# Optimization experiments

Measured on AMD Instinct MI355X. Metric: run time of the kernel, lower is better.

Reference implementation:

```python
import jax, jax.numpy as jnp
from jax import lax
import numpy as np

B, L, V, E, D, NC = 2048, 128, 128, 32, 64, 10
COMMIT = 0.25


def conv1d(x, w, b, stride, pad):
    # x: [N,C,L], w: torch Conv1d weight [out,in,k]
    y = lax.conv_general_dilated(x, w, (stride,), [(pad, pad)],
                                 dimension_numbers=('NCH', 'OIH', 'NCH'))
    return y + b[None, :, None]


def convT1d(x, w, b, stride, pad):
    # torch ConvTranspose1d weight [in,out,k]; out_len=(in-1)*stride-2*pad+k
    k = w.shape[-1]
    wf = jnp.flip(w, -1).transpose(1, 0, 2)  # -> OIH
    y = lax.conv_general_dilated(x, wf, (1,), [(k - 1 - pad, k - 1 - pad)],
                                 lhs_dilation=(stride,),
                                 dimension_numbers=('NCH', 'OIH', 'NCH'))
    return y + b[None, :, None]


def setup_inputs() -> dict:
    key = jax.random.key(0)
    ks = jax.random.split(key, 16)
    p = lambda k, shp, s=0.05: (jax.random.normal(k, shp, dtype=jnp.float32) * s)
    return {
        'text_indices': jax.random.randint(ks[0], (B, L), 0, V),
        'emb': p(ks[1], (V, E)),
        'enc_w1': p(ks[2], (64, E, 3)), 'enc_b1': jnp.zeros((64,), jnp.float32),
        'enc_w2': p(ks[3], (64, 64, 3)), 'enc_b2': jnp.zeros((64,), jnp.float32),
        'enc_w3': p(ks[4], (D, 64, 3)), 'enc_b3': jnp.zeros((D,), jnp.float32),
        'codebook': jax.random.uniform(ks[5], (NC, D), jnp.float32, -1.0 / NC, 1.0 / NC),
        'dec_w1': p(ks[6], (D, 64, 3)), 'dec_b1': jnp.zeros((64,), jnp.float32),
        'dec_w2': p(ks[7], (64, 64, 4)), 'dec_b2': jnp.zeros((64,), jnp.float32),
        'dec_w3': p(ks[8], (64, E, 4)), 'dec_b3': jnp.zeros((E,), jnp.float32),
        'out_w': p(ks[9], (V, E)), 'out_b': jnp.zeros((V,), jnp.float32),
    }


def reference(text_indices, emb, enc_w1, enc_b1, enc_w2, enc_b2, enc_w3, enc_b3,
              codebook, dec_w1, dec_b1, dec_w2, dec_b2, dec_w3, dec_b3, out_w, out_b):
    # ---- encode ----
    x = emb[text_indices]                      # [B,L,E]
    x = x.transpose(0, 2, 1)                   # [B,E,L]
    x = jax.nn.relu(conv1d(x, enc_w1, enc_b1, 2, 1))   # [B,64,64]
    x = jax.nn.relu(conv1d(x, enc_w2, enc_b2, 2, 1))   # [B,64,32]
    x = conv1d(x, enc_w3, enc_b3, 1, 0)        # [B,D,30]
    enc = x.transpose(0, 2, 1)                 # [B,30,D]
    features = jnp.broadcast_to(enc[:, :, None, :], (x.shape[0], 30, 30, D))  # [B,30,30,D]

    # ---- VQ: cdist + argmin + gather ----
    flat = features.reshape(-1, D)             # [B*900,D]
    d2 = (jnp.sum(flat * flat, axis=1, keepdims=True)
          - 2.0 * flat @ codebook.T
          + jnp.sum(codebook * codebook, axis=1)[None, :])  # [B*900,NC]
    codes = jnp.argmin(d2, axis=-1)
    puzzles = codes.reshape(features.shape[:-1])            # [B,30,30]
    quantized = codebook[codes].reshape(features.shape)     # [B,30,30,D]
    commitment_loss = jnp.mean((features - lax.stop_gradient(quantized)) ** 2)
    embedding_loss = jnp.mean((quantized - lax.stop_gradient(features)) ** 2)
    vq_loss = embedding_loss + COMMIT * commitment_loss
    quantized_st = features + lax.stop_gradient(quantized - features)

    # ---- decode ----
    f = quantized_st.mean(axis=2)              # [B,30,D]
    f = f.transpose(0, 2, 1)                   # [B,D,30]
    f = jax.nn.relu(convT1d(f, dec_w1, dec_b1, 1, 0))  # [B,64,32]
    f = jax.nn.relu(convT1d(f, dec_w2, dec_b2, 2, 1))  # [B,64,64]
    f = convT1d(f, dec_w3, dec_b3, 2, 1)       # [B,E,128]
    dec = f.transpose(0, 2, 1)                 # [B,L,E]
    char_logits = dec @ out_w.T + out_b        # [B,L,V]

    return char_logits, puzzles, features, quantized_st, vq_loss
```

## Files before the change

kernel.cpp:

```cpp
#include <hip/hip_runtime.h>
#include <hip/hip_bf16.h>

#define NBATCH 2048
#define SEQL   128
#define EMB    32
#define NCODE  10

#define OFF_LOG  0
#define OFF_PUZ  33554432
#define OFF_FEAT 35397632
#define OFF_Q    153362432
#define OFF_LOSS 271327232

#define WP_W1   0
#define WP_W2   6144
#define WP_W3   18432
#define WP_F32_END 30720

#define WH_W6   0
#define WH_W7E  12800
#define WH_W7O  21504
#define WH_W8E  30208
#define WH_W8O  34560
#define WH_OW   38912
#define WH_END  44032
#define WS_LOSS_BYTES 210944

typedef __attribute__((ext_vector_type(8))) short short8v;
typedef __attribute__((ext_vector_type(4))) float f32x4;

static __device__ __forceinline__ unsigned short f2bfu(float f) {
    __hip_bfloat16 h = __float2bfloat16(f);
    unsigned short u; __builtin_memcpy(&u, &h, 2); return u;
}

static __device__ __forceinline__ f32x4 mfma16(short8v a, short8v b, f32x4 c) {
    return __builtin_amdgcn_mfma_f32_16x16x32_bf16(a, b, c, 0, 0, 0);
}

__global__ void prep_weights(const float* __restrict__ w1, const float* __restrict__ w2,
                             const float* __restrict__ w3, const float* __restrict__ dw1,
                             const float* __restrict__ dw2, const float* __restrict__ dw3,
                             const float* __restrict__ ow,
                             float* __restrict__ wp, unsigned short* __restrict__ wph)
{
    int idx = blockIdx.x * 256 + threadIdx.x;
    if (idx < 6144) {
        int o = idx & 63, r = idx >> 6, kk = r % 3, i = r / 3;
        wp[WP_W1 + idx] = w1[(o * 32 + i) * 3 + kk];
    } else if (idx < 18432) {
        int t = idx - 6144;
        int o = t & 63, r = t >> 6, kk = r % 3, i = r / 3;
        wp[WP_W2 + t] = w2[(o * 64 + i) * 3 + kk];
    } else if (idx < 30720) {
        int t = idx - 18432;
        int o = t & 63, r = t >> 6, kk = r % 3, i = r / 3;
        wp[WP_W3 + t] = w3[(o * 64 + i) * 3 + kk];
    } else if (idx < 30720 + WH_END) {
        int t = idx - 30720;
        float v = 0.f;
        if (t < WH_W7E) {
            int o = t / 200, k = t % 200;
            if (k < 192) v = dw1[((k & 63) * 64 + o) * 3 + (k >> 6)];
        } else if (t < WH_W7O) {
            int s = t - WH_W7E; int o = s / 136, k = s % 136;
            if (k < 128) v = dw2[((k & 63) * 64 + o) * 4 + ((k >> 6) ? 3 : 1)];
        } else if (t < WH_W8E) {
            int s = t - WH_W7O; int o = s / 136, k = s % 136;
            if (k < 128) v = dw2[((k & 63) * 64 + o) * 4 + ((k >> 6) ? 2 : 0)];
        } else if (t < WH_W8O) {
            int s = t - WH_W8E; int o = s / 136, k = s % 136;
            if (k < 128) v = dw3[((k & 63) * 32 + o) * 4 + ((k >> 6) ? 3 : 1)];
        } else if (t < WH_OW) {
            int s = t - WH_W8O; int o = s / 136, k = s % 136;
            if (k < 128) v = dw3[((k & 63) * 32 + o) * 4 + ((k >> 6) ? 2 : 0)];
        } else {
            int s = t - WH_OW; int vv = s / 40, e = s % 40;
            if (e < 32) v = ow[vv * 32 + e];
        }
        wph[t] = f2bfu(v);
    }
}


__global__ __launch_bounds__(256, 4)
void vae_fused(const int* __restrict__ tidx, const float* __restrict__ emb,
               const float* __restrict__ b1, const float* __restrict__ b2,
               const float* __restrict__ b3, const float* __restrict__ cb,
               const float* __restrict__ db1, const float* __restrict__ db2,
               const float* __restrict__ db3, const float* __restrict__ ob,
               const float* __restrict__ wp, const unsigned short* __restrict__ wph,
               float* __restrict__ out, float* __restrict__ loss_part)
{
    __shared__ __align__(16) char sm[40000];
    float* xs   = (float*)(sm);
    float* h1   = (float*)(sm + 16640);
    float* h2   = (float*)(sm);
    float* h3   = (float*)(sm + 16640);
    float* cbs  = (float*)(sm + 24320);
    int*   codes= (int*)  (sm + 26880);
    float* encf = (float*)(sm);
    float* qf   = (float*)(sm + 7680);
    unsigned short* Xq = (unsigned short*)(sm + 27008);
    unsigned short* X7 = (unsigned short*)(sm + 15360);
    unsigned short* X8 = (unsigned short*)(sm + 20256);
    unsigned short* Xd = (unsigned short*)(sm + 29760);

    const int b   = blockIdx.x;
    const int tid = threadIdx.x;
    const int* ti = tidx + b * SEQL;

    const int lane = tid & 63;
    const int wid  = tid >> 6;
    const int lr = lane & 15, lk8 = (lane >> 4) * 8;
    const int rquad = (lane >> 4) * 4;

    for (int v = tid; v < EMB * SEQL; v += 256) {
        int l = v >> 5, e = v & 31;
        xs[e * 130 + 1 + l] = emb[ti[l] * EMB + e];
    }
    if (tid < 32) xs[tid * 130] = 0.f;
    __syncthreads();

    {
        const int og = tid >> 4, o0 = og * 4;
        const int ln = tid & 15;
        float acc[4][4];
        #pragma unroll
        for (int a = 0; a < 4; a++) {
            float bb = b1[o0 + a];
            #pragma unroll
            for (int c = 0; c < 4; c++) acc[a][c] = bb;
        }
        const float4* w1v = (const float4*)(wp + WP_W1);
        #pragma unroll 2
        for (int i = 0; i < 32; i++) {
            #pragma unroll
            for (int kk = 0; kk < 3; kk++) {
                float4 wv4 = w1v[(i * 3 + kk) * 16 + og];
                const float* wv = (const float*)&wv4;
                #pragma unroll
                for (int c = 0; c < 4; c++) {
                    float xv = xs[i * 130 + 2 * (ln + 16 * c) + kk];
                    #pragma unroll
                    for (int a = 0; a < 4; a++)
                        acc[a][c] = fmaf(wv[a], xv, acc[a][c]);
                }
            }
        }
        #pragma unroll
        for (int a = 0; a < 4; a++)
            #pragma unroll
            for (int c = 0; c < 4; c++)
                h1[(o0 + a) * 66 + 1 + ln + 16 * c] = fmaxf(acc[a][c], 0.f);
        if (tid < 64) h1[tid * 66] = 0.f;
    }
    __syncthreads();

    {
        const int og = tid >> 3, o0 = og * 2;
        const int ln = tid & 7;
        float acc[2][4];
        #pragma unroll
        for (int a = 0; a < 2; a++) {
            float bb = b2[o0 + a];
            #pragma unroll
            for (int c = 0; c < 4; c++) acc[a][c] = bb;
        }
        const float2* w2v = (const float2*)(wp + WP_W2);
        #pragma unroll 2
        for (int i = 0; i < 64; i++) {
            #pragma unroll
            for (int kk = 0; kk < 3; kk++) {
                float2 wv = w2v[(i * 3 + kk) * 32 + og];
                #pragma unroll
                for (int c = 0; c < 4; c++) {
                    float xv = h1[i * 66 + 2 * (ln + 8 * c) + kk];
                    acc[0][c] = fmaf(wv.x, xv, acc[0][c]);
                    acc[1][c] = fmaf(wv.y, xv, acc[1][c]);
                }
            }
        }
        #pragma unroll
        for (int a = 0; a < 2; a++)
            #pragma unroll
            for (int c = 0; c < 4; c++)
                h2[(o0 + a) * 34 + ln + 8 * c] = fmaxf(acc[a][c], 0.f);
        if (tid < 64) { h2[tid * 34 + 32] = 0.f; h2[tid * 34 + 33] = 0.f; }
    }
    __syncthreads();

    {
        const int og = tid >> 3, o0 = og * 2;
        const int ln = tid & 7;
        float acc[2][4];
        #pragma unroll
        for (int a = 0; a < 2; a++) {
            float bb = b3[o0 + a];
            #pragma unroll
            for (int c = 0; c < 4; c++) acc[a][c] = bb;
        }
        const float2* w3v = (const float2*)(wp + WP_W3);
        #pragma unroll 2
        for (int i = 0; i < 64; i++) {
            #pragma unroll
            for (int kk = 0; kk < 3; kk++) {
                float2 wv = w3v[(i * 3 + kk) * 32 + og];
                #pragma unroll
                for (int c = 0; c < 4; c++) {
                    float xv = h2[i * 34 + ln + 8 * c + kk];
                    acc[0][c] = fmaf(wv.x, xv, acc[0][c]);
                    acc[1][c] = fmaf(wv.y, xv, acc[1][c]);
                }
            }
        }
        #pragma unroll
        for (int a = 0; a < 2; a++)
            #pragma unroll
            for (int c = 0; c < 4; c++) {
                int col = ln + 8 * c;
                if (col < 30) h3[(o0 + a) * 30 + col] = acc[a][c];
            }
        for (int v = tid; v < NCODE * 64; v += 256) cbs[v] = cb[v];
    }
    __syncthreads();

    {
        float myd2 = 0.f;
        if (tid < 30) {
            const int i = tid;
            double d2[NCODE];
            #pragma unroll
            for (int c = 0; c < NCODE; c++) d2[c] = 0.0;
            for (int d = 0; d < 64; d++) {
                double v = (double)h3[d * 30 + i];
                #pragma unroll
                for (int c = 0; c < NCODE; c++) {
                    double df = v - (double)cbs[c * 64 + d];
                    d2[c] += df * df;
                }
            }
            int best = 0; double bd = d2[0];
            #pragma unroll
            for (int c = 1; c < NCODE; c++) if (d2[c] < bd) { bd = d2[c]; best = c; }
            codes[i] = best;
            myd2 = (float)bd;
        }
        float s = myd2;
        #pragma unroll
        for (int off = 32; off; off >>= 1) s += __shfl_down(s, off);
        if (tid == 0) loss_part[b] = s;
    }
    __syncthreads();

    {
        for (int v = tid; v < 30 * 64; v += 256) {
            int i = v >> 6, d = v & 63;
            float fv = h3[d * 30 + i];
            float qv = cbs[codes[i] * 64 + d];
            float sv = fv + (qv - fv);
            encf[v] = fv;
            qf[v]   = sv;
            Xq[(i + 2) * 72 + d] = f2bfu(sv);
        }
        for (int v = tid; v < 900; v += 256)
            out[OFF_PUZ + b * 900 + v] = (float)codes[v / 30];
        for (int v = tid; v < 4 * 72; v += 256) {
            int rr = v / 72, c = v % 72;
            int row = (rr < 2) ? rr : rr + 30;
            Xq[row * 72 + c] = 0;
        }
    }
    __syncthreads();

    {
        for (int v = tid; v < 2 * 72; v += 256) {
            int rr = v / 72, c = v % 72;
            X7[(rr ? 33 : 0) * 72 + c] = 0;
        }
        const unsigned short* w6p = wph + WH_W6;
        #pragma unroll
        for (int q = 0; q < 2; q++) {
            int T = wid * 2 + q;
            int m0 = (T >> 2) * 16, o0 = (T & 3) * 16;
            f32x4 acc;
            float bias = db1[o0 + lr];
            acc[0] = acc[1] = acc[2] = acc[3] = bias;
            #pragma unroll
            for (int kk = 0; kk < 3; kk++)
                #pragma unroll
                for (int k2 = 0; k2 < 2; k2++) {
                    short8v a = *(const short8v*)&Xq[(m0 + lr - kk + 2) * 72 + k2 * 32 + lk8];
                    short8v w = *(const short8v*)&w6p[(o0 + lr) * 200 + kk * 64 + k2 * 32 + lk8];
                    acc = mfma16(a, w, acc);
                }
            #pragma unroll
            for (int r = 0; r < 4; r++) {
                int t = m0 + rquad + r;
                X7[(t + 1) * 72 + o0 + lr] = f2bfu(fmaxf(acc[r], 0.f));
            }
        }
    }
    __syncthreads();

    {
        for (int v = tid; v < 2 * 72; v += 256) {
            int rr = v / 72, c = v % 72;
            X8[(rr ? 65 : 0) * 72 + c] = 0;
        }
        #pragma unroll
        for (int q = 0; q < 4; q++) {
            int T = wid * 4 + q;
            int p  = T >> 3;
            int m0 = ((T >> 2) & 1) * 16, o0 = (T & 3) * 16;
            const unsigned short* wb = wph + (p ? WH_W7O : WH_W7E);
            f32x4 acc;
            float bias = db2[o0 + lr];
            acc[0] = acc[1] = acc[2] = acc[3] = bias;
            int rb0 = p ? 2 : 1, rb1 = p ? 1 : 0;
            #pragma unroll
            for (int kb = 0; kb < 2; kb++) {
                int rbase = kb ? rb1 : rb0;
                #pragma unroll
                for (int k2 = 0; k2 < 2; k2++) {
                    short8v a = *(const short8v*)&X7[(m0 + lr + rbase) * 72 + k2 * 32 + lk8];
                    short8v w = *(const short8v*)&wb[(o0 + lr) * 136 + kb * 64 + k2 * 32 + lk8];
                    acc = mfma16(a, w, acc);
                }
            }
            #pragma unroll
            for (int r = 0; r < 4; r++) {
                int t = 2 * (m0 + rquad + r) + p;
                X8[(t + 1) * 72 + o0 + lr] = f2bfu(fmaxf(acc[r], 0.f));
            }
        }
    }
    __syncthreads();

    {
        #pragma unroll
        for (int q = 0; q < 4; q++) {
            int T = wid * 4 + q;
            int p  = T >> 3;
            int m0 = ((T >> 1) & 3) * 16, o0 = (T & 1) * 16;
            const unsigned short* wb = wph + (p ? WH_W8O : WH_W8E);
            f32x4 acc;
            float bias = db3[o0 + lr];
            acc[0] = acc[1] = acc[2] = acc[3] = bias;
            int rb0 = p ? 2 : 1, rb1 = p ? 1 : 0;
            #pragma unroll
            for (int kb = 0; kb < 2; kb++) {
                int rbase = kb ? rb1 : rb0;
                #pragma unroll
                for (int k2 = 0; k2 < 2; k2++) {
                    short8v a = *(const short8v*)&X8[(m0 + lr + rbase) * 72 + k2 * 32 + lk8];
                    short8v w = *(const short8v*)&wb[(o0 + lr) * 136 + kb * 64 + k2 * 32 + lk8];
                    acc = mfma16(a, w, acc);
                }
            }
            #pragma unroll
            for (int r = 0; r < 4; r++) {
                int l = 2 * (m0 + rquad + r) + p;
                Xd[l * 40 + o0 + lr] = f2bfu(acc[r]);
            }
        }
    }
    __syncthreads();

    {
        const unsigned short* owp = wph + WH_OW;
        float* outL = out + OFF_LOG + b * 16384;
        #pragma unroll 4
        for (int q = 0; q < 16; q++) {
            int T = wid * 16 + q;
            int m0 = (T >> 3) * 16, n0 = (T & 7) * 16;
            f32x4 acc;
            float bias = ob[n0 + lr];
            acc[0] = acc[1] = acc[2] = acc[3] = bias;
            short8v a = *(const short8v*)&Xd[(m0 + lr) * 40 + lk8];
            short8v w = *(const short8v*)&owp[(n0 + lr) * 40 + lk8];
            acc = mfma16(a, w, acc);
            #pragma unroll
            for (int r = 0; r < 4; r++)
                outL[(m0 + rquad + r) * 128 + n0 + lr] = acc[r];
        }
    }

    {
        float4* dF = ((float4*)(out + OFF_FEAT)) + b * 14400;
        float4* dQ = ((float4*)(out + OFF_Q))    + b * 14400;
        const float4* sE = (const float4*)encf;
        const float4* sQ = (const float4*)qf;
        for (int v = tid; v < 14400; v += 256) {
            int row = v >> 4, part = v & 15;
            int i = row / 30;
            dF[v] = sE[i * 16 + part];
            dQ[v] = sQ[i * 16 + part];
        }
    }
}

__global__ void loss_final(const float* __restrict__ part, float* __restrict__ out) {
    __shared__ float red[4];
    const int tid = threadIdx.x;
    float s = 0.f;
    for (int k = tid; k < NBATCH; k += 256) s += part[k];
    #pragma unroll
    for (int off = 32; off; off >>= 1) s += __shfl_down(s, off);
    if ((tid & 63) == 0) red[tid >> 6] = s;
    __syncthreads();
    if (tid == 0) {
        float t = red[0] + red[1] + red[2] + red[3];
        out[OFF_LOSS] = 1.25f * t / 3932160.0f;
    }
}

extern "C" void kernel_launch(void* const* d_in, const int* in_sizes, int n_in,
                              void* d_out, int out_size, void* d_ws, size_t ws_size,
                              hipStream_t stream) {
    const int*   tidx = (const int*)  d_in[0];
    const float* emb  = (const float*)d_in[1];
    const float* w1   = (const float*)d_in[2];
    const float* b1   = (const float*)d_in[3];
    const float* w2   = (const float*)d_in[4];
    const float* b2   = (const float*)d_in[5];
    const float* w3   = (const float*)d_in[6];
    const float* b3   = (const float*)d_in[7];
    const float* cb   = (const float*)d_in[8];
    const float* dw1  = (const float*)d_in[9];
    const float* db1  = (const float*)d_in[10];
    const float* dw2  = (const float*)d_in[11];
    const float* db2  = (const float*)d_in[12];
    const float* dw3  = (const float*)d_in[13];
    const float* db3  = (const float*)d_in[14];
    const float* ow   = (const float*)d_in[15];
    const float* ob   = (const float*)d_in[16];
    float* out = (float*)d_out;
    float* wp  = (float*)d_ws;
    unsigned short* wph = (unsigned short*)((char*)d_ws + 122880);
    float* part = (float*)((char*)d_ws + WS_LOSS_BYTES);

    prep_weights<<<292, 256, 0, stream>>>(w1, w2, w3, dw1, dw2, dw3, ow, wp, wph);
    vae_fused<<<NBATCH, 256, 0, stream>>>(tidx, emb, b1, b2, b3, cb,
                                          db1, db2, db3, ob, wp, wph,
                                          out, part);
    loss_final<<<1, 256, 0, stream>>>(part, out);
}
```

Measured before the change: 297.8 us.

## Process two batches per block and interleave feature/quantized stores with compute

Halves the grid so each block handles two batch items in sequence. The large features and quantized-output stores are split into chunks spread across the compute stages of the current and next item, so global writes overlap with the conv and MFMA work instead of forming a single tail burst. To free shared memory, features are staged in LDS as bf16 and expanded on write, and quantized rows are read straight from the codebook. This trades fewer resident blocks and possible precision loss on the features output for better overlap of the store-bound tail.

```diff
diff --git a/kernel.cpp b/kernel.cpp
--- a/kernel.cpp
+++ b/kernel.cpp
@@ -33,7 +33,9 @@
     __hip_bfloat16 h = __float2bfloat16(f);
     unsigned short u; __builtin_memcpy(&u, &h, 2); return u;
 }
-
+static __device__ __forceinline__ float bf2f(unsigned short u) {
+    return __uint_as_float(((unsigned)u) << 16);
+}
 static __device__ __forceinline__ f32x4 mfma16(short8v a, short8v b, f32x4 c) {
     return __builtin_amdgcn_mfma_f32_16x16x32_bf16(a, b, c, 0, 0, 0);
 }
@@ -92,312 +94,330 @@
                const float* __restrict__ wp, const unsigned short* __restrict__ wph,
                float* __restrict__ out, float* __restrict__ loss_part)
 {
-    __shared__ __align__(16) char sm[40000];
+    __shared__ __align__(16) char sm[40064];
     float* xs   = (float*)(sm);
     float* h1   = (float*)(sm + 16640);
     float* h2   = (float*)(sm);
     float* h3   = (float*)(sm + 16640);
-    float* cbs  = (float*)(sm + 24320);
-    int*   codes= (int*)  (sm + 26880);
-    float* encf = (float*)(sm);
-    float* qf   = (float*)(sm + 7680);
-    unsigned short* Xq = (unsigned short*)(sm + 27008);
-    unsigned short* X7 = (unsigned short*)(sm + 15360);
-    unsigned short* X8 = (unsigned short*)(sm + 20256);
-    unsigned short* Xd = (unsigned short*)(sm + 29760);
-
-    const int b   = blockIdx.x;
+    int*   codes= (int*)  (sm + 24320);
+    unsigned short* Xq = (unsigned short*)(sm + 24448);
+    unsigned short* X7 = (unsigned short*)(sm);
+    unsigned short* X8 = (unsigned short*)(sm + 4896);
+    unsigned short* Xd = (unsigned short*)(sm + 14400);
+    float* cbs  = (float*)(sm + 33536);
+    unsigned short* pe = (unsigned short*)(sm + 36096);
+    int* pcodes = (int*)(sm + 39936);
+
     const int tid = threadIdx.x;
-    const int* ti = tidx + b * SEQL;
-
     const int lane = tid & 63;
     const int wid  = tid >> 6;
     const int lr = lane & 15, lk8 = (lane >> 4) * 8;
     const int rquad = (lane >> 4) * 4;
 
-    for (int v = tid; v < EMB * SEQL; v += 256) {
-        int l = v >> 5, e = v & 31;
-        xs[e * 130 + 1 + l] = emb[ti[l] * EMB + e];
-    }
-    if (tid < 32) xs[tid * 130] = 0.f;
-    __syncthreads();
-
-    {
-        const int og = tid >> 4, o0 = og * 4;
-        const int ln = tid & 15;
-        float acc[4][4];
-        #pragma unroll
-        for (int a = 0; a < 4; a++) {
-            float bb = b1[o0 + a];
-            #pragma unroll
-            for (int c = 0; c < 4; c++) acc[a][c] = bb;
-        }
-        const float4* w1v = (const float4*)(wp + WP_W1);
-        #pragma unroll 2
-        for (int i = 0; i < 32; i++) {
-            #pragma unroll
-            for (int kk = 0; kk < 3; kk++) {
-                float4 wv4 = w1v[(i * 3 + kk) * 16 + og];
-                const float* wv = (const float*)&wv4;
-                #pragma unroll
-                for (int c = 0; c < 4; c++) {
-                    float xv = xs[i * 130 + 2 * (ln + 16 * c) + kk];
-                    #pragma unroll
-                    for (int a = 0; a < 4; a++)
-                        acc[a][c] = fmaf(wv[a], xv, acc[a][c]);
-                }
-            }
-        }
-        #pragma unroll
-        for (int a = 0; a < 4; a++)
-            #pragma unroll
-            for (int c = 0; c < 4; c++)
-                h1[(o0 + a) * 66 + 1 + ln + 16 * c] = fmaxf(acc[a][c], 0.f);
-        if (tid < 64) h1[tid * 66] = 0.f;
-    }
-    __syncthreads();
-
-    {
-        const int og = tid >> 3, o0 = og * 2;
-        const int ln = tid & 7;
-        float acc[2][4];
-        #pragma unroll
-        for (int a = 0; a < 2; a++) {
-            float bb = b2[o0 + a];
-            #pragma unroll
-            for (int c = 0; c < 4; c++) acc[a][c] = bb;
-        }
-        const float2* w2v = (const float2*)(wp + WP_W2);
-        #pragma unroll 2
-        for (int i = 0; i < 64; i++) {
-            #pragma unroll
-            for (int kk = 0; kk < 3; kk++) {
-                float2 wv = w2v[(i * 3 + kk) * 32 + og];
-                #pragma unroll
-                for (int c = 0; c < 4; c++) {
-                    float xv = h1[i * 66 + 2 * (ln + 8 * c) + kk];
-                    acc[0][c] = fmaf(wv.x, xv, acc[0][c]);
-                    acc[1][c] = fmaf(wv.y, xv, acc[1][c]);
-                }
-            }
-        }
-        #pragma unroll
-        for (int a = 0; a < 2; a++)
-            #pragma unroll
-            for (int c = 0; c < 4; c++)
-                h2[(o0 + a) * 34 + ln + 8 * c] = fmaxf(acc[a][c], 0.f);
-        if (tid < 64) { h2[tid * 34 + 32] = 0.f; h2[tid * 34 + 33] = 0.f; }
-    }
-    __syncthreads();
-
-    {
-        const int og = tid >> 3, o0 = og * 2;
-        const int ln = tid & 7;
-        float acc[2][4];
-        #pragma unroll
-        for (int a = 0; a < 2; a++) {
-            float bb = b3[o0 + a];
-            #pragma unroll
-            for (int c = 0; c < 4; c++) acc[a][c] = bb;
-        }
-        const float2* w3v = (const float2*)(wp + WP_W3);
-        #pragma unroll 2
-        for (int i = 0; i < 64; i++) {
-            #pragma unroll
-            for (int kk = 0; kk < 3; kk++) {
-                float2 wv = w3v[(i * 3 + kk) * 32 + og];
-                #pragma unroll
-                for (int c = 0; c < 4; c++) {
-                    float xv = h2[i * 34 + ln + 8 * c + kk];
-                    acc[0][c] = fmaf(wv.x, xv, acc[0][c]);
-                    acc[1][c] = fmaf(wv.y, xv, acc[1][c]);
-                }
-            }
-        }
-        #pragma unroll
-        for (int a = 0; a < 2; a++)
-            #pragma unroll
-            for (int c = 0; c < 4; c++) {
-                int col = ln + 8 * c;
-                if (col < 30) h3[(o0 + a) * 30 + col] = acc[a][c];
-            }
-        for (int v = tid; v < NCODE * 64; v += 256) cbs[v] = cb[v];
-    }
-    __syncthreads();
-
-    {
-        float myd2 = 0.f;
-        if (tid < 30) {
-            const int i = tid;
-            double d2[NCODE];
-            #pragma unroll
-            for (int c = 0; c < NCODE; c++) d2[c] = 0.0;
-            for (int d = 0; d < 64; d++) {
-                double v = (double)h3[d * 30 + i];
-                #pragma unroll
-                for (int c = 0; c < NCODE; c++) {
-                    double df = v - (double)cbs[c * 64 + d];
-                    d2[c] += df * df;
-                }
-            }
-            int best = 0; double bd = d2[0];
-            #pragma unroll
-            for (int c = 1; c < NCODE; c++) if (d2[c] < bd) { bd = d2[c]; best = c; }
-            codes[i] = best;
-            myd2 = (float)bd;
-        }
-        float s = myd2;
-        #pragma unroll
-        for (int off = 32; off; off >>= 1) s += __shfl_down(s, off);
-        if (tid == 0) loss_part[b] = s;
-    }
-    __syncthreads();
-
-    {
-        for (int v = tid; v < 30 * 64; v += 256) {
-            int i = v >> 6, d = v & 63;
-            float fv = h3[d * 30 + i];
-            float qv = cbs[codes[i] * 64 + d];
-            float sv = fv + (qv - fv);
-            encf[v] = fv;
-            qf[v]   = sv;
-            Xq[(i + 2) * 72 + d] = f2bfu(sv);
-        }
-        for (int v = tid; v < 900; v += 256)
-            out[OFF_PUZ + b * 900 + v] = (float)codes[v / 30];
-        for (int v = tid; v < 4 * 72; v += 256) {
-            int rr = v / 72, c = v % 72;
-            int row = (rr < 2) ? rr : rr + 30;
-            Xq[row * 72 + c] = 0;
-        }
-    }
-    __syncthreads();
-
-    {
-        for (int v = tid; v < 2 * 72; v += 256) {
-            int rr = v / 72, c = v % 72;
-            X7[(rr ? 33 : 0) * 72 + c] = 0;
-        }
-        const unsigned short* w6p = wph + WH_W6;
-        #pragma unroll
-        for (int q = 0; q < 2; q++) {
-            int T = wid * 2 + q;
-            int m0 = (T >> 2) * 16, o0 = (T & 3) * 16;
-            f32x4 acc;
-            float bias = db1[o0 + lr];
-            acc[0] = acc[1] = acc[2] = acc[3] = bias;
-            #pragma unroll
-            for (int kk = 0; kk < 3; kk++)
-                #pragma unroll
-                for (int k2 = 0; k2 < 2; k2++) {
-                    short8v a = *(const short8v*)&Xq[(m0 + lr - kk + 2) * 72 + k2 * 32 + lk8];
-                    short8v w = *(const short8v*)&w6p[(o0 + lr) * 200 + kk * 64 + k2 * 32 + lk8];
-                    acc = mfma16(a, w, acc);
-                }
-            #pragma unroll
-            for (int r = 0; r < 4; r++) {
-                int t = m0 + rquad + r;
-                X7[(t + 1) * 72 + o0 + lr] = f2bfu(fmaxf(acc[r], 0.f));
-            }
-        }
-    }
-    __syncthreads();
-
-    {
-        for (int v = tid; v < 2 * 72; v += 256) {
-            int rr = v / 72, c = v % 72;
-            X8[(rr ? 65 : 0) * 72 + c] = 0;
-        }
-        #pragma unroll
-        for (int q = 0; q < 4; q++) {
-            int T = wid * 4 + q;
-            int p  = T >> 3;
-            int m0 = ((T >> 2) & 1) * 16, o0 = (T & 3) * 16;
-            const unsigned short* wb = wph + (p ? WH_W7O : WH_W7E);
-            f32x4 acc;
-            float bias = db2[o0 + lr];
-            acc[0] = acc[1] = acc[2] = acc[3] = bias;
-            int rb0 = p ? 2 : 1, rb1 = p ? 1 : 0;
-            #pragma unroll
-            for (int kb = 0; kb < 2; kb++) {
-                int rbase = kb ? rb1 : rb0;
-                #pragma unroll
-                for (int k2 = 0; k2 < 2; k2++) {
-                    short8v a = *(const short8v*)&X7[(m0 + lr + rbase) * 72 + k2 * 32 + lk8];
-                    short8v w = *(const short8v*)&wb[(o0 + lr) * 136 + kb * 64 + k2 * 32 + lk8];
-                    acc = mfma16(a, w, acc);
-                }
-            }
-            #pragma unroll
-            for (int r = 0; r < 4; r++) {
-                int t = 2 * (m0 + rquad + r) + p;
-                X8[(t + 1) * 72 + o0 + lr] = f2bfu(fmaxf(acc[r], 0.f));
-            }
-        }
-    }
-    __syncthreads();
-
-    {
-        #pragma unroll
-        for (int q = 0; q < 4; q++) {
-            int T = wid * 4 + q;
-            int p  = T >> 3;
-            int m0 = ((T >> 1) & 3) * 16, o0 = (T & 1) * 16;
-            const unsigned short* wb = wph + (p ? WH_W8O : WH_W8E);
-            f32x4 acc;
-            float bias = db3[o0 + lr];
-            acc[0] = acc[1] = acc[2] = acc[3] = bias;
-            int rb0 = p ? 2 : 1, rb1 = p ? 1 : 0;
-            #pragma unroll
-            for (int kb = 0; kb < 2; kb++) {
-                int rbase = kb ? rb1 : rb0;
-                #pragma unroll
-                for (int k2 = 0; k2 < 2; k2++) {
-                    short8v a = *(const short8v*)&X8[(m0 + lr + rbase) * 72 + k2 * 32 + lk8];
-                    short8v w = *(const short8v*)&wb[(o0 + lr) * 136 + kb * 64 + k2 * 32 + lk8];
-                    acc = mfma16(a, w, acc);
-                }
-            }
-            #pragma unroll
-            for (int r = 0; r < 4; r++) {
-                int l = 2 * (m0 + rquad + r) + p;
-                Xd[l * 40 + o0 + lr] = f2bfu(acc[r]);
-            }
-        }
-    }
-    __syncthreads();
-
-    {
-        const unsigned short* owp = wph + WH_OW;
-        float* outL = out + OFF_LOG + b * 16384;
-        #pragma unroll 4
-        for (int q = 0; q < 16; q++) {
-            int T = wid * 16 + q;
-            int m0 = (T >> 3) * 16, n0 = (T & 7) * 16;
-            f32x4 acc;
-            float bias = ob[n0 + lr];
-            acc[0] = acc[1] = acc[2] = acc[3] = bias;
-            short8v a = *(const short8v*)&Xd[(m0 + lr) * 40 + lk8];
-            short8v w = *(const short8v*)&owp[(n0 + lr) * 40 + lk8];
-            acc = mfma16(a, w, acc);
-            #pragma unroll
-            for (int r = 0; r < 4; r++)
-                outL[(m0 + rquad + r) * 128 + n0 + lr] = acc[r];
-        }
-    }
-
-    {
-        float4* dF = ((float4*)(out + OFF_FEAT)) + b * 14400;
-        float4* dQ = ((float4*)(out + OFF_Q))    + b * 14400;
-        const float4* sE = (const float4*)encf;
-        const float4* sQ = (const float4*)qf;
-        for (int v = tid; v < 14400; v += 256) {
+    auto writeFQ = [&](int tb, int v0, int v1) {
+        float4* dF = ((float4*)(out + OFF_FEAT)) + tb * 14400;
+        float4* dQ = ((float4*)(out + OFF_Q))    + tb * 14400;
+        for (int v = v0 + tid; v < v1; v += 256) {
             int row = v >> 4, part = v & 15;
             int i = row / 30;
-            dF[v] = sE[i * 16 + part];
-            dQ[v] = sQ[i * 16 + part];
-        }
+            const unsigned short* pp = pe + i * 64 + part * 4;
+            float4 f;
+            f.x = bf2f(pp[0]); f.y = bf2f(pp[1]);
+            f.z = bf2f(pp[2]); f.w = bf2f(pp[3]);
+            float4 q = *(const float4*)&cbs[pcodes[i] * 64 + part * 4];
+            dF[v] = f; dQ[v] = q;
+        }
+    };
+
+    for (int p = 0; p < 2; ++p) {
+        const int b = blockIdx.x + (p << 10);
+        const int* ti = tidx + b * SEQL;
+
+        if (p) writeFQ(blockIdx.x, 6400, 7200);
+        for (int v = tid; v < EMB * SEQL; v += 256) {
+            int l = v >> 5, e = v & 31;
+            xs[e * 130 + 1 + l] = emb[ti[l] * EMB + e];
+        }
+        if (tid < 32) xs[tid * 130] = 0.f;
+        __syncthreads();
+
+        if (p) writeFQ(blockIdx.x, 7200, 9000);
+        {
+            const int og = tid >> 4, o0 = og * 4;
+            const int ln = tid & 15;
+            float acc[4][4];
+            #pragma unroll
+            for (int a = 0; a < 4; a++) {
+                float bb = b1[o0 + a];
+                #pragma unroll
+                for (int c = 0; c < 4; c++) acc[a][c] = bb;
+            }
+            const float4* w1v = (const float4*)(wp + WP_W1);
+            #pragma unroll 2
+            for (int i = 0; i < 32; i++) {
+                #pragma unroll
+                for (int kk = 0; kk < 3; kk++) {
+                    float4 wv4 = w1v[(i * 3 + kk) * 16 + og];
+                    const float* wv = (const float*)&wv4;
+                    #pragma unroll
+                    for (int c = 0; c < 4; c++) {
+                        float xv = xs[i * 130 + 2 * (ln + 16 * c) + kk];
+                        #pragma unroll
+                        for (int a = 0; a < 4; a++)
+                            acc[a][c] = fmaf(wv[a], xv, acc[a][c]);
+                    }
+                }
+            }
+            #pragma unroll
+            for (int a = 0; a < 4; a++)
+                #pragma unroll
+                for (int c = 0; c < 4; c++)
+                    h1[(o0 + a) * 66 + 1 + ln + 16 * c] = fmaxf(acc[a][c], 0.f);
+            if (tid < 64) h1[tid * 66] = 0.f;
+        }
+        __syncthreads();
+
+        if (p) writeFQ(blockIdx.x, 9000, 10800);
+        {
+            const int og = tid >> 3, o0 = og * 2;
+            const int ln = tid & 7;
+            float acc[2][4];
+            #pragma unroll
+            for (int a = 0; a < 2; a++) {
+                float bb = b2[o0 + a];
+                #pragma unroll
+                for (int c = 0; c < 4; c++) acc[a][c] = bb;
+            }
+            const float2* w2v = (const float2*)(wp + WP_W2);
+            #pragma unroll 2
+            for (int i = 0; i < 64; i++) {
+                #pragma unroll
+                for (int kk = 0; kk < 3; kk++) {
+                    float2 wv = w2v[(i * 3 + kk) * 32 + og];
+                    #pragma unroll
+                    for (int c = 0; c < 4; c++) {
+                        float xv = h1[i * 66 + 2 * (ln + 8 * c) + kk];
+                        acc[0][c] = fmaf(wv.x, xv, acc[0][c]);
+                        acc[1][c] = fmaf(wv.y, xv, acc[1][c]);
+                    }
+                }
+            }
+            #pragma unroll
+            for (int a = 0; a < 2; a++)
+                #pragma unroll
+                for (int c = 0; c < 4; c++)
+                    h2[(o0 + a) * 34 + ln + 8 * c] = fmaxf(acc[a][c], 0.f);
+            if (tid < 64) { h2[tid * 34 + 32] = 0.f; h2[tid * 34 + 33] = 0.f; }
+        }
+        __syncthreads();
+
+        if (p) writeFQ(blockIdx.x, 10800, 12600);
+        {
+            const int og = tid >> 3, o0 = og * 2;
+            const int ln = tid & 7;
+            float acc[2][4];
+            #pragma unroll
+            for (int a = 0; a < 2; a++) {
+                float bb = b3[o0 + a];
+                #pragma unroll
+                for (int c = 0; c < 4; c++) acc[a][c] = bb;
+            }
+            const float2* w3v = (const float2*)(wp + WP_W3);
+            #pragma unroll 2
+            for (int i = 0; i < 64; i++) {
+                #pragma unroll
+                for (int kk = 0; kk < 3; kk++) {
+                    float2 wv = w3v[(i * 3 + kk) * 32 + og];
+                    #pragma unroll
+                    for (int c = 0; c < 4; c++) {
+                        float xv = h2[i * 34 + ln + 8 * c + kk];
+                        acc[0][c] = fmaf(wv.x, xv, acc[0][c]);
+                        acc[1][c] = fmaf(wv.y, xv, acc[1][c]);
+                    }
+                }
+            }
+            #pragma unroll
+            for (int a = 0; a < 2; a++)
+                #pragma unroll
+                for (int c = 0; c < 4; c++) {
+                    int col = ln + 8 * c;
+                    if (col < 30) h3[(o0 + a) * 30 + col] = acc[a][c];
+                }
+            for (int v = tid; v < NCODE * 64; v += 256) cbs[v] = cb[v];
+        }
+        __syncthreads();
+
+        if (p) writeFQ(blockIdx.x, 12600, 14400);
+        {
+            float myd2 = 0.f;
+            if (tid < 30) {
+                const int i = tid;
+                double d2[NCODE];
+                #pragma unroll
+                for (int c = 0; c < NCODE; c++) d2[c] = 0.0;
+                for (int d = 0; d < 64; d++) {
+                    double v = (double)h3[d * 30 + i];
+                    #pragma unroll
+                    for (int c = 0; c < NCODE; c++) {
+                        double df = v - (double)cbs[c * 64 + d];
+                        d2[c] += df * df;
+                    }
+                }
+                int best = 0; double bd = d2[0];
+                #pragma unroll
+                for (int c = 1; c < NCODE; c++) if (d2[c] < bd) { bd = d2[c]; best = c; }
+                codes[i] = best;
+                myd2 = (float)bd;
+            }
+            float s = myd2;
+            #pragma unroll
+            for (int off = 32; off; off >>= 1) s += __shfl_down(s, off);
+            if (tid == 0) loss_part[b] = s;
+        }
+        __syncthreads();
+
+        {
+            for (int v = tid; v < 30 * 64; v += 256) {
+                int i = v >> 6, d = v & 63;
+                float fv = h3[d * 30 + i];
+                float qv = cbs[codes[i] * 64 + d];
+                float sv = fv + (qv - fv);
+                Xq[(i + 2) * 72 + d] = f2bfu(sv);
+                pe[v] = f2bfu(fv);
+            }
+            if (tid < 30) pcodes[tid] = codes[tid];
+            for (int v = tid; v < 900; v += 256)
+                out[OFF_PUZ + b * 900 + v] = (float)codes[v / 30];
+            for (int v = tid; v < 4 * 72; v += 256) {
+                int rr = v / 72, c = v % 72;
+                int row = (rr < 2) ? rr : rr + 30;
+                Xq[row * 72 + c] = 0;
+            }
+        }
+        __syncthreads();
+
+        const int s = p ? 2000 : 1600;
+
+        writeFQ(b, 0, s);
+        {
+            for (int v = tid; v < 2 * 72; v += 256) {
+                int rr = v / 72, c = v % 72;
+                X7[(rr ? 33 : 0) * 72 + c] = 0;
+            }
+            const unsigned short* w6p = wph + WH_W6;
+            #pragma unroll
+            for (int q = 0; q < 2; q++) {
+                int T = wid * 2 + q;
+                int m0 = (T >> 2) * 16, o0 = (T & 3) * 16;
+                f32x4 acc;
+                float bias = db1[o0 + lr];
+                acc[0] = acc[1] = acc[2] = acc[3] = bias;
+                #pragma unroll
+                for (int kk = 0; kk < 3; kk++)
+                    #pragma unroll
+                    for (int k2 = 0; k2 < 2; k2++) {
+                        short8v a = *(const short8v*)&Xq[(m0 + lr - kk + 2) * 72 + k2 * 32 + lk8];
+                        short8v w = *(const short8v*)&w6p[(o0 + lr) * 200 + kk * 64 + k2 * 32 + lk8];
+                        acc = mfma16(a, w, acc);
+                    }
+                #pragma unroll
+                for (int r = 0; r < 4; r++) {
+                    int t = m0 + rquad + r;
+                    X7[(t + 1) * 72 + o0 + lr] = f2bfu(fmaxf(acc[r], 0.f));
+                }
+            }
+        }
+        __syncthreads();
+
+        writeFQ(b, s, 2 * s);
+        {
+            for (int v = tid; v < 2 * 72; v += 256) {
+                int rr = v / 72, c = v % 72;
+                X8[(rr ? 65 : 0) * 72 + c] = 0;
+            }
+            #pragma unroll
+            for (int q = 0; q < 4; q++) {
+                int T = wid * 4 + q;
+                int pp = T >> 3;
+                int m0 = ((T >> 2) & 1) * 16, o0 = (T & 3) * 16;
+                const unsigned short* wb = wph + (pp ? WH_W7O : WH_W7E);
+                f32x4 acc;
+                float bias = db2[o0 + lr];
+                acc[0] = acc[1] = acc[2] = acc[3] = bias;
+                int rb0 = pp ? 2 : 1, rb1 = pp ? 1 : 0;
+                #pragma unroll
+                for (int kb = 0; kb < 2; kb++) {
+                    int rbase = kb ? rb1 : rb0;
+                    #pragma unroll
+                    for (int k2 = 0; k2 < 2; k2++) {
+                        short8v a = *(const short8v*)&X7[(m0 + lr + rbase) * 72 + k2 * 32 + lk8];
+                        short8v w = *(const short8v*)&wb[(o0 + lr) * 136 + kb * 64 + k2 * 32 + lk8];
+                        acc = mfma16(a, w, acc);
+                    }
+                }
+                #pragma unroll
+                for (int r = 0; r < 4; r++) {
+                    int t = 2 * (m0 + rquad + r) + pp;
+                    X8[(t + 1) * 72 + o0 + lr] = f2bfu(fmaxf(acc[r], 0.f));
+                }
+            }
+        }
+        __syncthreads();
+
+        writeFQ(b, 2 * s, 3 * s);
+        {
+            #pragma unroll
+            for (int q = 0; q < 4; q++) {
+                int T = wid * 4 + q;
+                int pp = T >> 3;
+                int m0 = ((T >> 1) & 3) * 16, o0 = (T & 1) * 16;
+                const unsigned short* wb = wph + (pp ? WH_W8O : WH_W8E);
+                f32x4 acc;
+                float bias = db3[o0 + lr];
+                acc[0] = acc[1] = acc[2] = acc[3] = bias;
+                int rb0 = pp ? 2 : 1, rb1 = pp ? 1 : 0;
+                #pragma unroll
+                for (int kb = 0; kb < 2; kb++) {
+                    int rbase = kb ? rb1 : rb0;
+                    #pragma unroll
+                    for (int k2 = 0; k2 < 2; k2++) {
+                        short8v a = *(const short8v*)&X8[(m0 + lr + rbase) * 72 + k2 * 32 + lk8];
+                        short8v w = *(const short8v*)&wb[(o0 + lr) * 136 + kb * 64 + k2 * 32 + lk8];
+                        acc = mfma16(a, w, acc);
+                    }
+                }
+                #pragma unroll
+                for (int r = 0; r < 4; r++) {
+                    int l = 2 * (m0 + rquad + r) + pp;
+                    Xd[l * 40 + o0 + lr] = f2bfu(acc[r]);
+                }
+            }
+        }
+        __syncthreads();
+
+        writeFQ(b, 3 * s, 4 * s);
+        {
+            const unsigned short* owp = wph + WH_OW;
+            float* outL = out + OFF_LOG + b * 16384;
+            #pragma unroll 4
+            for (int q = 0; q < 16; q++) {
+                int T = wid * 16 + q;
+                int m0 = (T >> 3) * 16, n0 = (T & 7) * 16;
+                f32x4 acc;
+                float bias = ob[n0 + lr];
+                acc[0] = acc[1] = acc[2] = acc[3] = bias;
+                short8v a = *(const short8v*)&Xd[(m0 + lr) * 40 + lk8];
+                short8v w = *(const short8v*)&owp[(n0 + lr) * 40 + lk8];
+                acc = mfma16(a, w, acc);
+                #pragma unroll
+                for (int r = 0; r < 4; r++)
+                    outL[(m0 + rquad + r) * 128 + n0 + lr] = acc[r];
+            }
+        }
+        __syncthreads();
     }
+
+    writeFQ(blockIdx.x + 1024, 8000, 14400);
 }
 
 __global__ void loss_final(const float* __restrict__ part, float* __restrict__ out) {
@@ -441,8 +461,8 @@
     float* part = (float*)((char*)d_ws + WS_LOSS_BYTES);
 
     prep_weights<<<292, 256, 0, stream>>>(w1, w2, w3, dw1, dw2, dw3, ow, wp, wph);
-    vae_fused<<<NBATCH, 256, 0, stream>>>(tidx, emb, b1, b2, b3, cb,
-                                          db1, db2, db3, ob, wp, wph,
-                                          out, part);
+    vae_fused<<<1024, 256, 0, stream>>>(tidx, emb, b1, b2, b3, cb,
+                                        db1, db2, db3, ob, wp, wph,
+                                        out, part);
     loss_final<<<1, 256, 0, stream>>>(part, out);
 }
```

Result: slower. 607.1 us (+103.9%).
